# Kernel tuning notes

Measured on AMD Instinct MI355X. Metric: run time of the kernel, lower is better.

The kernel has to match this reference:

```python
import jax, jax.numpy as jnp
import numpy as np

D_IN = 512
D_OUT = 512


def setup_inputs() -> dict:
    key = jax.random.key(0)
    ks = jax.random.split(key, 7)
    B, S = 4, 4096
    sc = 1.0 / np.sqrt(D_IN)
    return {
        "x": jax.random.normal(ks[0], (B, S, D_IN), dtype=jnp.float32),
        "Wq": jax.random.normal(ks[1], (D_IN, D_OUT), dtype=jnp.float32) * sc,
        "bq": jnp.zeros((D_OUT,), dtype=jnp.float32),
        "Wk": jax.random.normal(ks[2], (D_IN, D_OUT), dtype=jnp.float32) * sc,
        "bk": jnp.zeros((D_OUT,), dtype=jnp.float32),
        "Wv": jax.random.normal(ks[3], (D_IN, D_OUT), dtype=jnp.float32) * sc,
        "bv": jnp.zeros((D_OUT,), dtype=jnp.float32),
    }


def reference(x, Wq, bq, Wk, bk, Wv, bv):
    # Linear projections
    Q = x @ Wq + bq  # [B,S,Do]
    K = x @ Wk + bk
    V = x @ Wv + bv
    # NOTE: original torch code computes `len(K) ** 1 / 2` which is
    # (len(K)**1)/2 = batch_size / 2 due to operator precedence (not sqrt).
    scale = x.shape[0] / 2.0
    scores = jnp.einsum("bsd,btd->bst", Q, K) / scale  # [B,S,S]
    a = jax.nn.softmax(scores, axis=-1)
    Z = jnp.einsum("bst,btd->bsd", a, V)  # [B,S,Do]
    return Z
```

## Files before the change

kernel.cpp:

```cpp
#include <hip/hip_runtime.h>

typedef _Float16 h8 __attribute__((ext_vector_type(8)));
typedef float f4 __attribute__((ext_vector_type(4)));

#define MFMA16(a, b, c) __builtin_amdgcn_mfma_f32_16x16x32_f16((a), (b), (c), 0, 0, 0)

__device__ static inline void gl_lds16(const void* g, void* l) {
  __builtin_amdgcn_global_load_lds((const __attribute__((address_space(1))) unsigned int*)g,
                                   (__attribute__((address_space(3))) unsigned int*)l, 16, 0, 0);
}

__device__ static inline unsigned encf(float f) {
  unsigned u = __float_as_uint(f);
  return (u & 0x80000000u) ? ~u : (u | 0x80000000u);
}
__device__ static inline float decf(unsigned u) {
  return __uint_as_float((u & 0x80000000u) ? (u ^ 0x80000000u) : ~u);
}


__global__ void wconv_kernel(const float* __restrict__ Wq, const float* __restrict__ Wk,
                             const float* __restrict__ Wv, _Float16* __restrict__ Wt,
                             unsigned* __restrict__ mEnc) {
  int idx = blockIdx.x * 256 + threadIdx.x;
  if (idx < 16384) mEnc[idx] = 0u;
  int z = idx >> 15, rem = idx & 32767;
  int n = rem >> 6, k0 = (rem & 63) << 3;
  const float* W = (z == 0) ? Wq : (z == 1) ? Wk : Wv;
  float sc = (z == 0) ? 0.5f : 1.0f;
  h8 v;
#pragma unroll
  for (int j = 0; j < 8; ++j) v[j] = (_Float16)(W[(k0 + j) * 512 + n] * sc);
  size_t blk = (size_t)((z * 4 + (n >> 7)) * 8 + (k0 >> 6));
  int off = (n & 127) * 64 + ((((k0 >> 3) & 7) ^ (n & 7)) << 3);
  *(h8*)&Wt[blk * 8192 + off] = v;
}

__global__ __launch_bounds__(256, 3)
void proj_kernel(const float* __restrict__ x, const _Float16* __restrict__ Wt,
                 const float* __restrict__ bq, const float* __restrict__ bk,
                 const float* __restrict__ bv,
                 char* __restrict__ Qimg, char* __restrict__ Kimg, char* __restrict__ VTimg) {
  __shared__ _Float16 sMem[16384];
  _Float16* sA = sMem;
  _Float16* sB = sMem + 8192;
  const int tid = threadIdx.x;
  const int wave = tid >> 6, lane = tid & 63;
  const int quad = lane >> 4, lr = lane & 15;
  const int mbase = blockIdx.x * 128, nbase = blockIdx.y * 128, z = blockIdx.z;
  const int sr = tid >> 1, sseg = tid & 1;
  const int rbase = (wave & 1) * 64, cbase = (wave >> 1) * 64;
  const char* WtB = (const char*)Wt + ((size_t)(z * 4 + (nbase >> 7)) * 8) * 16384;

  float4 ax[8];
  f4 acc[4][4];
#pragma unroll
  for (int i = 0; i < 4; ++i)
#pragma unroll
    for (int j = 0; j < 4; ++j) { f4 zz = {0.f, 0.f, 0.f, 0.f}; acc[i][j] = zz; }

  {
    const float4* asrc = (const float4*)&x[(size_t)(mbase + sr) * 512 + sseg * 32];
#pragma unroll
    for (int i = 0; i < 8; ++i) ax[i] = asrc[i];
#pragma unroll
    for (int j = 0; j < 4; ++j)
      gl_lds16(WtB + tid * 16 + j * 4096, (char*)sB + tid * 16 + j * 4096);
  }

  for (int kt = 0; kt < 8; ++kt) {
    if (kt > 0) __syncthreads();
#pragma unroll
    for (int i = 0; i < 4; ++i) {
      h8 v;
      float4 f0 = ax[2 * i], f1 = ax[2 * i + 1];
      v[0] = (_Float16)f0.x; v[1] = (_Float16)f0.y; v[2] = (_Float16)f0.z; v[3] = (_Float16)f0.w;
      v[4] = (_Float16)f1.x; v[5] = (_Float16)f1.y; v[6] = (_Float16)f1.z; v[7] = (_Float16)f1.w;
      *(h8*)&sA[sr * 64 + (((sseg * 4 + i) ^ (sr & 7)) << 3)] = v;
    }
    if (kt > 0) {
#pragma unroll
      for (int j = 0; j < 4; ++j)
        gl_lds16(WtB + kt * 16384 + tid * 16 + j * 4096, (char*)sB + tid * 16 + j * 4096);
    }
    __syncthreads();
    if (kt < 7) {
      const float4* asrc = (const float4*)&x[(size_t)(mbase + sr) * 512 + (kt + 1) * 64 + sseg * 32];
#pragma unroll
      for (int i = 0; i < 8; ++i) ax[i] = asrc[i];
    }
#pragma unroll
    for (int ks = 0; ks < 2; ++ks) {
      h8 a[4], bb[4];
#pragma unroll
      for (int rt = 0; rt < 4; ++rt) {
        const int r = rbase + rt * 16 + lr;
        a[rt] = *(const h8*)&sA[r * 64 + ((((ks << 2) | quad) ^ (lr & 7)) << 3)];
      }
#pragma unroll
      for (int ct = 0; ct < 4; ++ct) {
        const int r = cbase + ct * 16 + lr;
        bb[ct] = *(const h8*)&sB[r * 64 + ((((ks << 2) | quad) ^ (lr & 7)) << 3)];
      }
#pragma unroll
      for (int rt = 0; rt < 4; ++rt)
#pragma unroll
        for (int ct = 0; ct < 4; ++ct)
          acc[rt][ct] = MFMA16(a[rt], bb[ct], acc[rt][ct]);
    }
  }

  const float* bias = (z == 0) ? bq : (z == 1) ? bk : bv;
  const float bscale = (z == 0) ? 0.5f : 1.0f;
  _Float16* sC = sMem;
  __syncthreads();
#pragma unroll
  for (int ct = 0; ct < 4; ++ct) {
    const int dl = cbase + ct * 16 + lr;
    const float bb = bias[nbase + dl] * bscale;
#pragma unroll
    for (int rt = 0; rt < 4; ++rt) {
#pragma unroll
      for (int r = 0; r < 4; ++r) {
        const int sl = rbase + rt * 16 + quad * 4 + r;
        const _Float16 val = (_Float16)(acc[rt][ct][r] + bb);
        if (z == 2) {
          sC[((sl >> 6) << 13) + dl * 64 + ((((sl >> 3) & 7) ^ (dl & 7)) << 3) + (sl & 7)] = val;
        } else {
          sC[((dl >> 6) << 13) + sl * 64 + ((((dl >> 3) & 7) ^ (sl & 7)) << 3) + (dl & 7)] = val;
        }
      }
    }
  }
  __syncthreads();
  const int b_ = mbase >> 12;
  char* dst;
  if (z != 2) {
    char* img = (z == 0) ? Qimg : Kimg;
    dst = img + ((size_t)((b_ * 32 + ((mbase & 4095) >> 7)) * 8 + (nbase >> 6) + (tid >> 7))) * 16384;
  } else {
    dst = VTimg + ((size_t)((b_ * 4 + (nbase >> 7)) * 64 + ((mbase & 4095) >> 6) + (tid >> 7))) * 16384;
  }
  dst += (size_t)(tid & 127) * 128;
#pragma unroll
  for (int k = 0; k < 8; ++k)
    *(int4*)(dst + k * 16) = *(const int4*)&sC[tid * 64 + k * 8];
}

__global__ __launch_bounds__(256, 3)
void qk_kernel(const char* __restrict__ Qimg, const char* __restrict__ Kimg,
               char* __restrict__ S, unsigned* __restrict__ mEnc, int b0, int s0) {
  __shared__ _Float16 sMem[16384];
  _Float16* sA = sMem;
  _Float16* sB = sMem + 8192;
  const int tid = threadIdx.x;
  const int wave = tid >> 6, lane = tid & 63;
  const int quad = lane >> 4, lr = lane & 15;
  const int cb = blockIdx.x;
  const int rbL = blockIdx.z * gridDim.y + blockIdx.y;
  const int b = b0 + blockIdx.z;
  const int rbase = (wave & 1) * 64, cbase = (wave >> 1) * 64;
  const char* Ab = Qimg + ((size_t)((b * 32 + (s0 >> 7) + blockIdx.y) * 8)) * 16384;
  const char* Bb = Kimg + ((size_t)((b * 32 + cb) * 8)) * 16384;

  f4 acc[4][4];
#pragma unroll
  for (int i = 0; i < 4; ++i)
#pragma unroll
    for (int j = 0; j < 4; ++j) { f4 zz = {0.f, 0.f, 0.f, 0.f}; acc[i][j] = zz; }

#pragma unroll
  for (int j = 0; j < 4; ++j) {
    gl_lds16(Ab + tid * 16 + j * 4096, (char*)sA + tid * 16 + j * 4096);
    gl_lds16(Bb + tid * 16 + j * 4096, (char*)sB + tid * 16 + j * 4096);
  }

  for (int kt = 0; kt < 8; ++kt) {
    __syncthreads();
#pragma unroll
    for (int ks = 0; ks < 2; ++ks) {
      h8 a[4], bb[4];
#pragma unroll
      for (int rt = 0; rt < 4; ++rt) {
        const int r = rbase + rt * 16 + lr;
        a[rt] = *(const h8*)&sA[r * 64 + ((((ks << 2) | quad) ^ (lr & 7)) << 3)];
      }
#pragma unroll
      for (int ct = 0; ct < 4; ++ct) {
        const int r = cbase + ct * 16 + lr;
        bb[ct] = *(const h8*)&sB[r * 64 + ((((ks << 2) | quad) ^ (lr & 7)) << 3)];
      }
#pragma unroll
      for (int rt = 0; rt < 4; ++rt)
#pragma unroll
        for (int ct = 0; ct < 4; ++ct)
          acc[rt][ct] = MFMA16(a[rt], bb[ct], acc[rt][ct]);
    }
    __syncthreads();
    if (kt < 7) {
#pragma unroll
      for (int j = 0; j < 4; ++j) {
        gl_lds16(Ab + (kt + 1) * 16384 + tid * 16 + j * 4096, (char*)sA + tid * 16 + j * 4096);
        gl_lds16(Bb + (kt + 1) * 16384 + tid * 16 + j * 4096, (char*)sB + tid * 16 + j * 4096);
      }
    }
  }

  {
    const int growb = b * 4096 + s0 + blockIdx.y * 128;
#pragma unroll
    for (int rt = 0; rt < 4; ++rt) {
#pragma unroll
      for (int r = 0; r < 4; ++r) {
        float mx = fmaxf(fmaxf(acc[rt][0][r], acc[rt][1][r]),
                         fmaxf(acc[rt][2][r], acc[rt][3][r]));
        mx = fmaxf(mx, __shfl_xor(mx, 1));
        mx = fmaxf(mx, __shfl_xor(mx, 2));
        mx = fmaxf(mx, __shfl_xor(mx, 4));
        mx = fmaxf(mx, __shfl_xor(mx, 8));
        if (lr == 0)
          atomicMax(&mEnc[growb + rbase + rt * 16 + quad * 4 + r], encf(mx));
      }
    }
  }

  _Float16* sC = sMem;
#pragma unroll
  for (int ct = 0; ct < 4; ++ct) {
    const int tl = cbase + ct * 16 + lr;
#pragma unroll
    for (int rt = 0; rt < 4; ++rt) {
#pragma unroll
      for (int r = 0; r < 4; ++r) {
        const int sl = rbase + rt * 16 + quad * 4 + r;
        sC[((tl >> 6) << 13) + sl * 64 + ((((tl >> 3) & 7) ^ (sl & 7)) << 3) + (tl & 7)] =
            (_Float16)acc[rt][ct][r];
      }
    }
  }
  __syncthreads();
  char* dst = S + ((size_t)(rbL * 64 + cb * 2 + (tid >> 7))) * 16384 + (size_t)(tid & 127) * 128;
#pragma unroll
  for (int k = 0; k < 8; ++k)
    *(int4*)(dst + k * 16) = *(const int4*)&sC[tid * 64 + k * 8];
}

__global__ __launch_bounds__(256, 4)
void pv_kernel(const char* __restrict__ S, const char* __restrict__ VTimg,
               const unsigned* __restrict__ mEnc, float* __restrict__ out, int b0, int s0) {
  __shared__ _Float16 sMem[12288];
  __shared__ float ls[64];
  _Float16* sA = sMem;
  _Float16* sB = sMem + 4096;
  const int tid = threadIdx.x;
  const int wave = tid >> 6, lane = tid & 63;
  const int quad = lane >> 4, lr = lane & 15;
  const int db = blockIdx.x;
  const int sbL = blockIdx.z * gridDim.y + blockIdx.y;
  const int b = b0 + blockIdx.z;
  const int rbase = (wave & 1) * 32, cbase = (wave >> 1) * 64;
  const char* Ab = S + ((size_t)((sbL >> 1) * 64)) * 16384 + (size_t)(sbL & 1) * 8192;
  const char* Bb = VTimg + ((size_t)((b * 4 + db) * 64)) * 16384;

  const int lrow = tid >> 3;
  const int growb = b * 4096 + s0 + blockIdx.y * 64;
  const float m0 = decf(mEnc[growb + lrow]);
  const float m1 = decf(mEnc[growb + 32 + lrow]);
  float rs0 = 0.f, rs1 = 0.f;

  f4 acc[2][4];
#pragma unroll
  for (int i = 0; i < 2; ++i)
#pragma unroll
    for (int j = 0; j < 4; ++j) { f4 zz = {0.f, 0.f, 0.f, 0.f}; acc[i][j] = zz; }

  {
#pragma unroll
    for (int j = 0; j < 4; ++j)
      gl_lds16(Bb + tid * 16 + j * 4096, (char*)sB + tid * 16 + j * 4096);
    {
      h8 ha = *(const h8*)(Ab + tid * 16);
      h8 w;
#pragma unroll
      for (int u = 0; u < 8; ++u) { float e = __expf((float)ha[u] - m0); w[u] = (_Float16)e; rs0 += e; }
      *(h8*)((char*)sA + tid * 16) = w;
    }
    {
      h8 ha = *(const h8*)(Ab + tid * 16 + 4096);
      h8 w;
#pragma unroll
      for (int u = 0; u < 8; ++u) { float e = __expf((float)ha[u] - m1); w[u] = (_Float16)e; rs1 += e; }
      *(h8*)((char*)sA + tid * 16 + 4096) = w;
    }
  }

  for (int kt = 0; kt < 64; ++kt) {
    __syncthreads();
#pragma unroll
    for (int ks = 0; ks < 2; ++ks) {
      h8 a[2], bb[4];
#pragma unroll
      for (int rt = 0; rt < 2; ++rt) {
        const int r = rbase + rt * 16 + lr;
        a[rt] = *(const h8*)&sA[r * 64 + ((((ks << 2) | quad) ^ (lr & 7)) << 3)];
      }
#pragma unroll
      for (int ct = 0; ct < 4; ++ct) {
        const int r = cbase + ct * 16 + lr;
        bb[ct] = *(const h8*)&sB[r * 64 + ((((ks << 2) | quad) ^ (lr & 7)) << 3)];
      }
#pragma unroll
      for (int rt = 0; rt < 2; ++rt)
#pragma unroll
        for (int ct = 0; ct < 4; ++ct)
          acc[rt][ct] = MFMA16(a[rt], bb[ct], acc[rt][ct]);
    }
    __syncthreads();
    if (kt < 63) {
#pragma unroll
      for (int j = 0; j < 4; ++j)
        gl_lds16(Bb + (kt + 1) * 16384 + tid * 16 + j * 4096, (char*)sB + tid * 16 + j * 4096);
      {
        h8 ha = *(const h8*)(Ab + (kt + 1) * 16384 + tid * 16);
        h8 w;
#pragma unroll
        for (int u = 0; u < 8; ++u) { float e = __expf((float)ha[u] - m0); w[u] = (_Float16)e; rs0 += e; }
        *(h8*)((char*)sA + tid * 16) = w;
      }
      {
        h8 ha = *(const h8*)(Ab + (kt + 1) * 16384 + tid * 16 + 4096);
        h8 w;
#pragma unroll
        for (int u = 0; u < 8; ++u) { float e = __expf((float)ha[u] - m1); w[u] = (_Float16)e; rs1 += e; }
        *(h8*)((char*)sA + tid * 16 + 4096) = w;
      }
    }
  }

  rs0 += __shfl_xor(rs0, 1); rs0 += __shfl_xor(rs0, 2); rs0 += __shfl_xor(rs0, 4);
  rs1 += __shfl_xor(rs1, 1); rs1 += __shfl_xor(rs1, 2); rs1 += __shfl_xor(rs1, 4);
  if ((tid & 7) == 0) { ls[lrow] = rs0; ls[32 + lrow] = rs1; }
  __syncthreads();

#pragma unroll
  for (int rt = 0; rt < 2; ++rt) {
#pragma unroll
    for (int r = 0; r < 4; ++r) {
      const int lrw = rbase + rt * 16 + quad * 4 + r;
      const int srow = s0 + blockIdx.y * 64 + lrw;
      const float li = 1.0f / ls[lrw];
      float* op = &out[((size_t)b * 4096 + srow) * 512 + db * 128];
#pragma unroll
      for (int ct = 0; ct < 4; ++ct)
        op[cbase + ct * 16 + lr] = acc[rt][ct][r] * li;
    }
  }
}

extern "C" void kernel_launch(void* const* d_in, const int* in_sizes, int n_in,
                              void* d_out, int out_size, void* d_ws, size_t ws_size,
                              hipStream_t stream) {
  (void)in_sizes; (void)n_in; (void)out_size;
  const float* x  = (const float*)d_in[0];
  const float* Wq = (const float*)d_in[1];
  const float* bq = (const float*)d_in[2];
  const float* Wk = (const float*)d_in[3];
  const float* bk = (const float*)d_in[4];
  const float* Wv = (const float*)d_in[5];
  const float* bv = (const float*)d_in[6];
  float* out = (float*)d_out;
  char* ws = (char*)d_ws;
  char* Qimg  = ws;
  char* Kimg  = ws + ((size_t)16 << 20);
  char* VTimg = ws + ((size_t)32 << 20);
  _Float16* Wt = (_Float16*)(ws + ((size_t)48 << 20));
  unsigned* mEnc = (unsigned*)(ws + ((size_t)50 << 20) - 65536);
  char* Simg   = ws + ((size_t)50 << 20);

  wconv_kernel<<<dim3(384), dim3(256), 0, stream>>>(Wq, Wk, Wv, Wt, mEnc);
  proj_kernel<<<dim3(128, 4, 3), dim3(256), 0, stream>>>(x, Wt, bq, bk, bv, Qimg, Kimg, VTimg);

  const size_t avail = ws_size > ((size_t)50 << 20) ? ws_size - ((size_t)50 << 20) : 0;
  int nchunk, nb, Ms;
  if      (avail >= ((size_t)128 << 20)) { nchunk = 1;  nb = 4; Ms = 4096; }
  else if (avail >= ((size_t)64  << 20)) { nchunk = 2;  nb = 2; Ms = 4096; }
  else if (avail >= ((size_t)32  << 20)) { nchunk = 4;  nb = 1; Ms = 4096; }
  else if (avail >= ((size_t)16  << 20)) { nchunk = 8;  nb = 1; Ms = 2048; }
  else if (avail >= ((size_t)8   << 20)) { nchunk = 16; nb = 1; Ms = 1024; }
  else                                   { nchunk = 32; nb = 1; Ms = 512;  }
  const int chunksPerBatch = 4096 / Ms;

  for (int c = 0; c < nchunk; ++c) {
    int b0, s0;
    if (nb > 1 || Ms == 4096) { b0 = c * nb; s0 = 0; }
    else { b0 = c / chunksPerBatch; s0 = (c % chunksPerBatch) * Ms; }
    qk_kernel<<<dim3(32, Ms / 128, nb), dim3(256), 0, stream>>>(Qimg, Kimg, Simg, mEnc, b0, s0);
    pv_kernel<<<dim3(4, Ms / 64, nb), dim3(256), 0, stream>>>(Simg, VTimg, mEnc, out, b0, s0);
  }
}
```

Before: 375.9 us.

## Overlap next-tile loads with MFMA by reading LDS to registers before barrier

Both the score GEMM and the PV GEMM loops now load the full tile's LDS fragments into registers, barrier, then issue the next tile's global-to-LDS loads (and exp conversion) before running the MFMAs. This lets memory traffic for tile k+1 proceed while tile k is being computed, where before the loads started only after the compute finished. The MFMA blocks are wrapped in raised wave priority. The global read of the next A tile is hoisted ahead of the barrier so its latency is hidden. In exchange, register pressure rises from holding both k-slices of fragments, and the exp work now sits between the barrier and the MFMAs.

New measurement: 405.1 us. 7.8% more time.

```diff
diff --git a/kernel.cpp b/kernel.cpp
--- a/kernel.cpp
+++ b/kernel.cpp
@@ -176,27 +176,26 @@
   }
 
   for (int kt = 0; kt < 8; ++kt) {
-    __syncthreads();
+    asm volatile("s_waitcnt vmcnt(0)" ::: "memory");
+    __builtin_amdgcn_s_barrier();
+    __builtin_amdgcn_sched_barrier(0);
+    h8 a[4][2], bb[4][2];
 #pragma unroll
     for (int ks = 0; ks < 2; ++ks) {
-      h8 a[4], bb[4];
 #pragma unroll
       for (int rt = 0; rt < 4; ++rt) {
         const int r = rbase + rt * 16 + lr;
-        a[rt] = *(const h8*)&sA[r * 64 + ((((ks << 2) | quad) ^ (lr & 7)) << 3)];
+        a[rt][ks] = *(const h8*)&sA[r * 64 + ((((ks << 2) | quad) ^ (lr & 7)) << 3)];
       }
 #pragma unroll
       for (int ct = 0; ct < 4; ++ct) {
         const int r = cbase + ct * 16 + lr;
-        bb[ct] = *(const h8*)&sB[r * 64 + ((((ks << 2) | quad) ^ (lr & 7)) << 3)];
-      }
-#pragma unroll
-      for (int rt = 0; rt < 4; ++rt)
-#pragma unroll
-        for (int ct = 0; ct < 4; ++ct)
-          acc[rt][ct] = MFMA16(a[rt], bb[ct], acc[rt][ct]);
-    }
-    __syncthreads();
+        bb[ct][ks] = *(const h8*)&sB[r * 64 + ((((ks << 2) | quad) ^ (lr & 7)) << 3)];
+      }
+    }
+    asm volatile("s_waitcnt lgkmcnt(0)" ::: "memory");
+    __builtin_amdgcn_s_barrier();
+    __builtin_amdgcn_sched_barrier(0);
     if (kt < 7) {
 #pragma unroll
       for (int j = 0; j < 4; ++j) {
@@ -204,6 +203,15 @@
         gl_lds16(Bb + (kt + 1) * 16384 + tid * 16 + j * 4096, (char*)sB + tid * 16 + j * 4096);
       }
     }
+    __builtin_amdgcn_s_setprio(1);
+#pragma unroll
+    for (int ks = 0; ks < 2; ++ks)
+#pragma unroll
+      for (int rt = 0; rt < 4; ++rt)
+#pragma unroll
+        for (int ct = 0; ct < 4; ++ct)
+          acc[rt][ct] = MFMA16(a[rt][ks], bb[ct][ks], acc[rt][ct]);
+    __builtin_amdgcn_s_setprio(0);
   }
 
   {
@@ -225,6 +233,7 @@
   }
 
   _Float16* sC = sMem;
+  __syncthreads();
 #pragma unroll
   for (int ct = 0; ct < 4; ++ct) {
     const int tl = cbase + ct * 16 + lr;
@@ -295,46 +304,52 @@
   }
 
   for (int kt = 0; kt < 64; ++kt) {
-    __syncthreads();
+    asm volatile("s_waitcnt vmcnt(0) lgkmcnt(0)" ::: "memory");
+    __builtin_amdgcn_s_barrier();
+    __builtin_amdgcn_sched_barrier(0);
+    h8 a[2][2], bb[4][2];
 #pragma unroll
     for (int ks = 0; ks < 2; ++ks) {
-      h8 a[2], bb[4];
 #pragma unroll
       for (int rt = 0; rt < 2; ++rt) {
         const int r = rbase + rt * 16 + lr;
-        a[rt] = *(const h8*)&sA[r * 64 + ((((ks << 2) | quad) ^ (lr & 7)) << 3)];
+        a[rt][ks] = *(const h8*)&sA[r * 64 + ((((ks << 2) | quad) ^ (lr & 7)) << 3)];
       }
 #pragma unroll
       for (int ct = 0; ct < 4; ++ct) {
         const int r = cbase + ct * 16 + lr;
-        bb[ct] = *(const h8*)&sB[r * 64 + ((((ks << 2) | quad) ^ (lr & 7)) << 3)];
-      }
-#pragma unroll
-      for (int rt = 0; rt < 2; ++rt)
-#pragma unroll
-        for (int ct = 0; ct < 4; ++ct)
-          acc[rt][ct] = MFMA16(a[rt], bb[ct], acc[rt][ct]);
-    }
-    __syncthreads();
+        bb[ct][ks] = *(const h8*)&sB[r * 64 + ((((ks << 2) | quad) ^ (lr & 7)) << 3)];
+      }
+    }
+    h8 ha0, ha1;
+    if (kt < 63) {
+      ha0 = *(const h8*)(Ab + (kt + 1) * 16384 + tid * 16);
+      ha1 = *(const h8*)(Ab + (kt + 1) * 16384 + tid * 16 + 4096);
+    }
+    asm volatile("s_waitcnt lgkmcnt(0)" ::: "memory");
+    __builtin_amdgcn_s_barrier();
+    __builtin_amdgcn_sched_barrier(0);
     if (kt < 63) {
 #pragma unroll
       for (int j = 0; j < 4; ++j)
         gl_lds16(Bb + (kt + 1) * 16384 + tid * 16 + j * 4096, (char*)sB + tid * 16 + j * 4096);
-      {
-        h8 ha = *(const h8*)(Ab + (kt + 1) * 16384 + tid * 16);
-        h8 w;
-#pragma unroll
-        for (int u = 0; u < 8; ++u) { float e = __expf((float)ha[u] - m0); w[u] = (_Float16)e; rs0 += e; }
-        *(h8*)((char*)sA + tid * 16) = w;
-      }
-      {
-        h8 ha = *(const h8*)(Ab + (kt + 1) * 16384 + tid * 16 + 4096);
-        h8 w;
-#pragma unroll
-        for (int u = 0; u < 8; ++u) { float e = __expf((float)ha[u] - m1); w[u] = (_Float16)e; rs1 += e; }
-        *(h8*)((char*)sA + tid * 16 + 4096) = w;
-      }
-    }
+      h8 w0, w1;
+#pragma unroll
+      for (int u = 0; u < 8; ++u) { float e = __expf((float)ha0[u] - m0); w0[u] = (_Float16)e; rs0 += e; }
+#pragma unroll
+      for (int u = 0; u < 8; ++u) { float e = __expf((float)ha1[u] - m1); w1[u] = (_Float16)e; rs1 += e; }
+      *(h8*)((char*)sA + tid * 16) = w0;
+      *(h8*)((char*)sA + tid * 16 + 4096) = w1;
+    }
+    __builtin_amdgcn_s_setprio(1);
+#pragma unroll
+    for (int ks = 0; ks < 2; ++ks)
+#pragma unroll
+      for (int rt = 0; rt < 2; ++rt)
+#pragma unroll
+        for (int ct = 0; ct < 4; ++ct)
+          acc[rt][ct] = MFMA16(a[rt][ks], bb[ct][ks], acc[rt][ct]);
+    __builtin_amdgcn_s_setprio(0);
   }
 
   rs0 += __shfl_xor(rs0, 1); rs0 += __shfl_xor(rs0, 2); rs0 += __shfl_xor(rs0, 4);
```
